# Optimization experiments

Hardware: AMD Instinct MI355X
Metric: run time of the kernel (lower is better)

The kernel has to match this reference:

```python
import jax, jax.numpy as jnp
import numpy as np

_EPS = 1e-5

def _bn(x, g, t, m, v):
    # inference-mode BatchNorm (channels-last)
    return g * (x - m) * jax.lax.rsqrt(v + _EPS) + t

def _lin(x, w, b):
    # 1x1 conv == linear over last (channel) axis; w: (out, in)
    return jnp.einsum('...c,oc->...o', x, w) + b

def _forward(points, k, c0_w, c0_b, c0_g, c0_t, c0_m, c0_v,
             c1_w, c1_b, c1_g, c1_t, c1_m, c1_v,
             a0_w, a0_b, a0_g, a0_t, a0_m, a0_v,
             a1_w, a1_b, a1_g, a1_t, a1_m, a1_v,
             a2_w, a2_b, a2_g, a2_t, a2_m, a2_v,
             c2_w, c2_b, c2_g, c2_t, c2_m, c2_v,
             c3_w, c3_b, c3_g, c3_t, c3_m, c3_v,
             c4_w, c4_b):
    B, N, _ = points.shape
    # per-point MLP: 3 -> 64 -> 64
    x = jax.nn.relu(_bn(_lin(points, c0_w, c0_b), c0_g, c0_t, c0_m, c0_v))
    x = jax.nn.relu(_bn(_lin(x, c1_w, c1_b), c1_g, c1_t, c1_m, c1_v))
    # kNN via squared distances (same ordering as cdist); idx: (B,N,k)
    sq = jnp.sum(points * points, axis=-1)  # (B,N)
    d = sq[:, :, None] + sq[:, None, :] - 2.0 * jnp.einsum('bnc,bmc->bnm', points, points)
    idx = jax.lax.top_k(-d, k)[1]  # (B,N,k) smallest distances
    bidx = jnp.arange(B)[:, None, None]
    grouped_xyz = points[bidx, idx] - points[:, :, None, :]  # (B,N,k,3), centered
    grouped_pts = x[bidx, idx]                                # (B,N,k,64)
    g = jnp.concatenate([grouped_xyz, grouped_pts], axis=-1)  # (B,N,k,67)
    # per-neighbor MLP 67 -> 64 -> 128 -> 128
    for (w, b, ga, t, m, v) in ((a0_w, a0_b, a0_g, a0_t, a0_m, a0_v),
                                (a1_w, a1_b, a1_g, a1_t, a1_m, a1_v),
                                (a2_w, a2_b, a2_g, a2_t, a2_m, a2_v)):
        g = jax.nn.relu(_bn(_lin(g, w, b), ga, t, m, v))
    local = jnp.max(g, axis=2)                 # (B,N,128) max over k neighbors
    gf = jnp.max(local, axis=1, keepdims=True)  # (B,1,128) global feature
    feat = jnp.concatenate([local, jnp.broadcast_to(gf, local.shape)], axis=-1)  # (B,N,256)
    feat = jax.nn.relu(_bn(_lin(feat, c2_w, c2_b), c2_g, c2_t, c2_m, c2_v))
    feat = jax.nn.relu(_bn(_lin(feat, c3_w, c3_b), c3_g, c3_t, c3_m, c3_v))
    # dropout is identity in eval mode
    return _lin(feat, c4_w, c4_b)  # (B,N,6)

def setup_inputs() -> dict:
    key = jax.random.key(0)
    B, N, K = 8, 4096, 16
    specs = [("c0", 64, 3, True), ("c1", 64, 64, True), ("a0", 64, 67, True),
             ("a1", 128, 64, True), ("a2", 128, 128, True), ("c2", 256, 256, True),
             ("c3", 128, 256, True), ("c4", 6, 128, False)]
    inp = {"points": jax.random.normal(key, (B, N, 3), jnp.float32)}
    i = 0
    for name, o, c, has_bn in specs:
        i += 1
        kw = jax.random.fold_in(key, i)
        inp[name + "_w"] = jax.random.normal(kw, (o, c), jnp.float32) * 0.05
        inp[name + "_b"] = jnp.zeros((o,), jnp.float32)
        if has_bn:
            inp[name + "_g"] = jnp.ones((o,), jnp.float32)
            inp[name + "_t"] = jnp.zeros((o,), jnp.float32)
            inp[name + "_m"] = jax.random.normal(jax.random.fold_in(kw, 1), (o,), jnp.float32) * 0.05
            inp[name + "_v"] = jnp.ones((o,), jnp.float32)
    inp["k"] = K
    return inp

def reference(points, c0_w, c0_b, c0_g, c0_t, c0_m, c0_v,
              c1_w, c1_b, c1_g, c1_t, c1_m, c1_v,
              a0_w, a0_b, a0_g, a0_t, a0_m, a0_v,
              a1_w, a1_b, a1_g, a1_t, a1_m, a1_v,
              a2_w, a2_b, a2_g, a2_t, a2_m, a2_v,
              c2_w, c2_b, c2_g, c2_t, c2_m, c2_v,
              c3_w, c3_b, c3_g, c3_t, c3_m, c3_v,
              c4_w, c4_b, k):
    return _forward(points, k, c0_w, c0_b, c0_g, c0_t, c0_m, c0_v,
                    c1_w, c1_b, c1_g, c1_t, c1_m, c1_v,
                    a0_w, a0_b, a0_g, a0_t, a0_m, a0_v,
                    a1_w, a1_b, a1_g, a1_t, a1_m, a1_v,
                    a2_w, a2_b, a2_g, a2_t, a2_m, a2_v,
                    c2_w, c2_b, c2_g, c2_t, c2_m, c2_v,
                    c3_w, c3_b, c3_g, c3_t, c3_m, c3_v,
                    c4_w, c4_b)
```

## Files before the change

### kernel.cpp

```cpp
#include <hip/hip_runtime.h>
#include <math.h>


#define EPSBN 1e-5f

typedef _Float16 v8h  __attribute__((ext_vector_type(8)));
typedef _Float16 v4h  __attribute__((ext_vector_type(4)));
typedef float    v16f __attribute__((ext_vector_type(16)));

#define W0T_OFF   0
#define B0_OFF    192
#define W1T_OFF   256
#define B1_OFF    4352
#define A0XT_OFF  4416
#define A0FT_OFF  4608
#define BA0_OFF   8704
#define A1T_OFF   8768
#define BA1_OFF   16960
#define A2T_OFF   17088
#define BA2_OFF   33472
#define C2T_OFF   33600
#define C3H_OFF   66368
#define BC2_OFF   99136
#define BC3_OFF   132160
#define C4T_OFF   132288
#define BC4_OFF   133056
#define PTS4_OFF  133120
#define Q_OFF     264192
#define C_OFF     2361344
#define IDX_OFF   4458496
#define LOCAL_OFF 4982784
#define GF_OFF    9177088

__device__ __forceinline__ void fold_one(int e, const float* w, const float* b,
    const float* g, const float* t, const float* m, const float* v,
    float* wt, float* bo, int O, int Cfull, int cbeg)
{
    int o = e % O, c = e / O;
    float s = 1.0f;
    if (g) s = g[o] * (1.0f / sqrtf(v[o] + EPSBN));
    wt[c * O + o] = w[o * Cfull + cbeg + c] * s;
    if (c == 0 && bo) {
        float bias = b[o];
        if (g) bias = (bias - m[o]) * s + t[o];
        bo[o] = bias;
    }
}

__global__ __launch_bounds__(256) void fold_kernel(
    const float* c0w, const float* c0b, const float* c0g, const float* c0t, const float* c0m, const float* c0v,
    const float* c1w, const float* c1b, const float* c1g, const float* c1t, const float* c1m, const float* c1v,
    const float* a0w, const float* a0b, const float* a0g, const float* a0t, const float* a0m, const float* a0v,
    const float* a1w, const float* a1b, const float* a1g, const float* a1t, const float* a1m, const float* a1v,
    const float* a2w, const float* a2b, const float* a2g, const float* a2t, const float* a2m, const float* a2v,
    const float* c2w, const float* c2b, const float* c2g, const float* c2t, const float* c2m, const float* c2v,
    const float* c3w, const float* c3b, const float* c3g, const float* c3t, const float* c3m, const float* c3v,
    const float* c4w, const float* c4b,
    float* ws)
{
    int e = blockIdx.x * 256 + threadIdx.x;
    if (e < 192)        { fold_one(e,          c0w, c0b, c0g, c0t, c0m, c0v, ws + W0T_OFF,  ws + B0_OFF,  64, 3,   0); return; }
    e -= 192;
    if (e < 4096)       { fold_one(e,          c1w, c1b, c1g, c1t, c1m, c1v, ws + W1T_OFF,  ws + B1_OFF,  64, 64,  0); return; }
    e -= 4096;
    if (e < 192)        { fold_one(e,          a0w, a0b, a0g, a0t, a0m, a0v, ws + A0XT_OFF, ws + BA0_OFF, 64, 67,  0); return; }
    e -= 192;
    if (e < 4096)       { fold_one(e,          a0w, a0b, a0g, a0t, a0m, a0v, ws + A0FT_OFF, nullptr,      64, 67,  3); return; }
    e -= 4096;
    if (e < 8192) {
        int j = e & 7, l = (e >> 3) & 63, kf = (e >> 9) & 3, wv = e >> 11;
        int o = wv * 32 + (l & 31);
        int c = kf * 16 + (l >> 5) * 8 + j;
        float s = a1g[o] * (1.0f / sqrtf(a1v[o] + EPSBN));
        ((_Float16*)(ws + A1T_OFF))[e] = (_Float16)(a1w[o * 64 + c] * s);
        if (c == 0) ws[BA1_OFF + o] = (a1b[o] - a1m[o]) * s + a1t[o];
        return;
    }
    e -= 8192;
    if (e < 16384) {
        int j = e & 7, l = (e >> 3) & 63, kf = (e >> 9) & 7, wv = e >> 12;
        int o = wv * 32 + (l & 31);
        int c = kf * 16 + (l >> 5) * 8 + j;
        float s = a2g[o] * (1.0f / sqrtf(a2v[o] + EPSBN));
        ((_Float16*)(ws + A2T_OFF))[e] = (_Float16)(a2w[o * 128 + c] * s);
        if (c == 0) ws[BA2_OFF + o] = (a2b[o] - a2m[o]) * s + a2t[o];
        return;
    }
    e -= 16384;
    if (e < 65536) {
        int j = e & 7, l = (e >> 3) & 63, s5 = (e >> 9) & 15, ot = e >> 13;
        int o = ot * 32 + (l & 31);
        int c = s5 * 16 + (l >> 5) * 8 + j;
        float sc = c2g[o] * (1.0f / sqrtf(c2v[o] + EPSBN));
        ((_Float16*)(ws + C2T_OFF))[e] = (_Float16)(c2w[o * 256 + c] * sc);
        if (c == 0) ws[BC2_OFF + o] = (c2b[o] - c2m[o]) * sc + c2t[o];
        return;
    }
    e -= 65536;
    if (e < 32768) {
        int j = e & 7, l = (e >> 3) & 63, s5 = (e >> 9) & 15, ot = e >> 13;
        int o = ot * 32 + (l & 31);
        int c = s5 * 16 + (l >> 5) * 8 + j;
        float sc = c3g[o] * (1.0f / sqrtf(c3v[o] + EPSBN));
        ((_Float16*)(ws + C3H_OFF))[e] = (_Float16)(c3w[o * 256 + c] * sc);
        if (c == 0) ws[BC3_OFF + o] = (c3b[o] - c3m[o]) * sc + c3t[o];
        return;
    }
    e -= 32768;
    if (e < 768)        { fold_one(e,          c4w, c4b, nullptr, nullptr, nullptr, nullptr, ws + C4T_OFF, ws + BC4_OFF, 6, 128, 0); return; }
    e -= 768;
    if (e < 1024)       { ws[GF_OFF + e] = 0.0f; return; }
}

__global__ __launch_bounds__(256) void point_mlp_kernel(const float* __restrict__ pts, float* __restrict__ ws)
{
    __shared__ float sh[4][64][4];
    __shared__ float sx[4][64][4];
    int lane = threadIdx.x & 63;
    int wv = threadIdx.x >> 6;
    int pid0 = blockIdx.x * 16 + wv * 4;

    const float* pc = pts + (size_t)pid0 * 3;
    float c0x = pc[0], c0y = pc[1],  c0z = pc[2];
    float c1x = pc[3], c1y = pc[4],  c1z = pc[5];
    float c2x = pc[6], c2y = pc[7],  c2z = pc[8];
    float c3x = pc[9], c3y = pc[10], c3z = pc[11];

    if (lane < 4) {
        const float* pp = pts + (size_t)(pid0 + lane) * 3;
        float xx = pp[0], yy = pp[1], zz = pp[2];
        float sq = __fadd_rn(__fadd_rn(__fmul_rn(xx, xx), __fmul_rn(yy, yy)), __fmul_rn(zz, zz));
        ((float4*)(ws + PTS4_OFF))[pid0 + lane] = make_float4(xx, yy, zz, sq);
    }

    const float* W0T  = ws + W0T_OFF;
    const float* B0   = ws + B0_OFF;
    const float* W1T  = ws + W1T_OFF;
    const float* B1   = ws + B1_OFF;
    const float* A0XT = ws + A0XT_OFF;
    const float* A0FT = ws + A0FT_OFF;
    const float* BA0  = ws + BA0_OFF;

    float b0 = B0[lane];
    float w0a = W0T[lane], w0b = W0T[64 + lane], w0c = W0T[128 + lane];
    float4 h;
    h.x = fmaxf(fmaf(c0z, w0c, fmaf(c0y, w0b, fmaf(c0x, w0a, b0))), 0.0f);
    h.y = fmaxf(fmaf(c1z, w0c, fmaf(c1y, w0b, fmaf(c1x, w0a, b0))), 0.0f);
    h.z = fmaxf(fmaf(c2z, w0c, fmaf(c2y, w0b, fmaf(c2x, w0a, b0))), 0.0f);
    h.w = fmaxf(fmaf(c3z, w0c, fmaf(c3y, w0b, fmaf(c3x, w0a, b0))), 0.0f);
    *(float4*)&sh[wv][lane][0] = h;

    float b1v = B1[lane];
    float a0 = b1v, a1 = b1v, a2 = b1v, a3 = b1v;
    #pragma unroll 8
    for (int c = 0; c < 64; ++c) {
        float w = W1T[c * 64 + lane];
        float4 hv = *(const float4*)&sh[wv][c][0];
        a0 = fmaf(w, hv.x, a0);
        a1 = fmaf(w, hv.y, a1);
        a2 = fmaf(w, hv.z, a2);
        a3 = fmaf(w, hv.w, a3);
    }
    float4 xv;
    xv.x = fmaxf(a0, 0.0f);
    xv.y = fmaxf(a1, 0.0f);
    xv.z = fmaxf(a2, 0.0f);
    xv.w = fmaxf(a3, 0.0f);
    *(float4*)&sx[wv][lane][0] = xv;

    float ax = A0XT[lane], ay = A0XT[64 + lane], az = A0XT[128 + lane];
    float q0 = __fmul_rn(c0x, ax); q0 = fmaf(c0y, ay, q0); q0 = fmaf(c0z, az, q0);
    float q1 = __fmul_rn(c1x, ax); q1 = fmaf(c1y, ay, q1); q1 = fmaf(c1z, az, q1);
    float q2 = __fmul_rn(c2x, ax); q2 = fmaf(c2y, ay, q2); q2 = fmaf(c2z, az, q2);
    float q3 = __fmul_rn(c3x, ax); q3 = fmaf(c3y, ay, q3); q3 = fmaf(c3z, az, q3);
    ws[Q_OFF + (size_t)(pid0 + 0) * 64 + lane] = q0;
    ws[Q_OFF + (size_t)(pid0 + 1) * 64 + lane] = q1;
    ws[Q_OFF + (size_t)(pid0 + 2) * 64 + lane] = q2;
    ws[Q_OFF + (size_t)(pid0 + 3) * 64 + lane] = q3;

    float ba = BA0[lane];
    float e0 = q0 + ba, e1 = q1 + ba, e2 = q2 + ba, e3 = q3 + ba;
    #pragma unroll 8
    for (int c = 0; c < 64; ++c) {
        float w = A0FT[c * 64 + lane];
        float4 sv = *(const float4*)&sx[wv][c][0];
        e0 = fmaf(w, sv.x, e0);
        e1 = fmaf(w, sv.y, e1);
        e2 = fmaf(w, sv.z, e2);
        e3 = fmaf(w, sv.w, e3);
    }
    ws[C_OFF + (size_t)(pid0 + 0) * 64 + lane] = e0;
    ws[C_OFF + (size_t)(pid0 + 1) * 64 + lane] = e1;
    ws[C_OFF + (size_t)(pid0 + 2) * 64 + lane] = e2;
    ws[C_OFF + (size_t)(pid0 + 3) * 64 + lane] = e3;
}

__device__ __forceinline__ float dist2_ref(float xn, float yn, float zn, float sqn, float4 pm)
{
    float dot = __fmul_rn(xn, pm.x);
    dot = __fmaf_rn(yn, pm.y, dot);
    dot = __fmaf_rn(zn, pm.z, dot);
    float s = __fadd_rn(sqn, pm.w);
    return __fmaf_rn(-2.0f, dot, s);
}

__device__ __forceinline__ float dtilde(float xn, float yn, float zn, float4 pm)
{
    float dot = __fmul_rn(xn, pm.x);
    dot = __fmaf_rn(yn, pm.y, dot);
    dot = __fmaf_rn(zn, pm.z, dot);
    return __fmaf_rn(-2.0f, dot, pm.w);
}

#define KNN_CAP 64
#define KNN_MARGIN 1e-3f

__device__ __forceinline__ void knn_row(
    const float4* __restrict__ pts4, int* __restrict__ IDX,
    float* __restrict__ bufdW, int* __restrict__ bufiW, int* __restrict__ cntp,
    int base, int rbase, int rw, int l, float gm, float tvd)
{
    unsigned long long qm = __ballot(gm <= tvd);

    float4 pr = pts4[rbase + rw];
    float xr = pr.x, yr = pr.y, zr = pr.z, sr = pr.w;
    float tve = __fadd_rn(sr, tvd);

    int cr = 0;
    #define KNN_PROC(GG, CV)                                                   \
    {                                                                          \
        float d = dist2_ref(xr, yr, zr, sr, (CV));                             \
        bool p = (d <= tve);                                                   \
        unsigned long long mk = __ballot(p);                                   \
        int my = __builtin_amdgcn_mbcnt_hi((unsigned)(mk >> 32),               \
                 __builtin_amdgcn_mbcnt_lo((unsigned)mk, 0));                  \
        int slot = cr + my;                                                    \
        if (p && slot < KNN_CAP) { bufdW[slot] = d; bufiW[slot] = (GG) * 64 + l; } \
        cr += (int)__popcll(mk);                                               \
    }
    while (qm) {
        int g0 = __ffsll((unsigned long long)qm) - 1; qm &= qm - 1;
        int g1 = -1, g2 = -1, g3 = -1;
        if (qm) { g1 = __ffsll((unsigned long long)qm) - 1; qm &= qm - 1;
            if (qm) { g2 = __ffsll((unsigned long long)qm) - 1; qm &= qm - 1;
                if (qm) { g3 = __ffsll((unsigned long long)qm) - 1; qm &= qm - 1; } } }
        float4 cv0 = pts4[base + g0 * 64 + l];
        float4 cv1, cv2, cv3;
        if (g1 >= 0) cv1 = pts4[base + g1 * 64 + l];
        if (g2 >= 0) cv2 = pts4[base + g2 * 64 + l];
        if (g3 >= 0) cv3 = pts4[base + g3 * 64 + l];
        KNN_PROC(g0, cv0);
        if (g1 >= 0) KNN_PROC(g1, cv1);
        if (g2 >= 0) KNN_PROC(g2, cv2);
        if (g3 >= 0) KNN_PROC(g3, cv3);
    }
    #undef KNN_PROC
    if (l == 0) *cntp = cr;

    if (cr <= KNN_CAP) {
        unsigned long long key = ~0ULL;
        if (l < cr) {
            unsigned u = __float_as_uint(bufdW[l]);
            u = (u & 0x80000000u) ? ~u : (u | 0x80000000u);
            key = ((unsigned long long)u << 32) | (unsigned)bufiW[l];
        }
        if (cr <= 32) {
            #pragma unroll
            for (int k = 2; k <= 32; k <<= 1) {
                #pragma unroll
                for (int j = k >> 1; j > 0; j >>= 1) {
                    unsigned long long o = __shfl_xor(key, j);
                    bool mx = (((l & j) != 0) == ((l & k) == 0));
                    key = mx ? (key > o ? key : o) : (key < o ? key : o);
                }
            }
        } else {
            #pragma unroll
            for (int k = 2; k <= 64; k <<= 1) {
                #pragma unroll
                for (int j = k >> 1; j > 0; j >>= 1) {
                    unsigned long long o = __shfl_xor(key, j);
                    bool mx = (((l & j) != 0) == ((l & k) == 0));
                    key = mx ? (key > o ? key : o) : (key < o ? key : o);
                }
            }
        }
        if (l < 16)
            IDX[(rbase + rw) * 16 + l] = (int)(key & 0xFFFFFFFFu);
    }
}

__global__ __launch_bounds__(1024) void knn_kernel(float* __restrict__ ws)
{
    __shared__ float gmins[64 * 65];
    __shared__ float bufd[16][72];
    __shared__ int   bufi[16][72];
    __shared__ int   cnt[64];

    const float4* __restrict__ pts4 = (const float4*)(ws + PTS4_OFF);
    int* IDX = (int*)(ws + IDX_OFF);

    const int l     = threadIdx.x & 63;
    const int row   = l;
    const int wvu   = __builtin_amdgcn_readfirstlane(threadIdx.x >> 6);
    const int base  = (blockIdx.x >> 6) << 12;
    const int rbase = blockIdx.x * 64;
    const int r     = rbase + row;

    float4 pn = pts4[r];
    float xn = pn.x, yn = pn.y, zn = pn.z, sqn = pn.w;
    (void)sqn;

    #pragma unroll
    for (int g = 0; g < 4; ++g) {
        const float4* __restrict__ cp = pts4 + base + wvu * 256 + g * 64;
        float mn0 = INFINITY, mn1 = INFINITY, mn2 = INFINITY, mn3 = INFINITY;
        #pragma unroll 4
        for (int i = 0; i < 64; i += 4) {
            mn0 = fminf(mn0, dtilde(xn, yn, zn, cp[i + 0]));
            mn1 = fminf(mn1, dtilde(xn, yn, zn, cp[i + 1]));
            mn2 = fminf(mn2, dtilde(xn, yn, zn, cp[i + 2]));
            mn3 = fminf(mn3, dtilde(xn, yn, zn, cp[i + 3]));
        }
        gmins[row * 65 + wvu * 4 + g] = fminf(fminf(mn0, mn1), fminf(mn2, mn3));
    }
    __syncthreads();

    float gm0 = gmins[(wvu * 4 + 0) * 65 + l];
    float gm1 = gmins[(wvu * 4 + 1) * 65 + l];
    float gm2 = gmins[(wvu * 4 + 2) * 65 + l];
    float gm3 = gmins[(wvu * 4 + 3) * 65 + l];
    float v0 = gm0, v1 = gm1, v2 = gm2, v3 = gm3;
    #pragma unroll
    for (int k = 2; k <= 64; k <<= 1) {
        #pragma unroll
        for (int j = k >> 1; j > 0; j >>= 1) {
            float o0 = __shfl_xor(v0, j);
            float o1 = __shfl_xor(v1, j);
            float o2 = __shfl_xor(v2, j);
            float o3 = __shfl_xor(v3, j);
            bool mx = (((l & j) != 0) == ((l & k) == 0));
            v0 = mx ? fmaxf(v0, o0) : fminf(v0, o0);
            v1 = mx ? fmaxf(v1, o1) : fminf(v1, o1);
            v2 = mx ? fmaxf(v2, o2) : fminf(v2, o2);
            v3 = mx ? fmaxf(v3, o3) : fminf(v3, o3);
        }
    }
    float tvd0 = __shfl(v0, 16) + KNN_MARGIN;
    float tvd1 = __shfl(v1, 16) + KNN_MARGIN;
    float tvd2 = __shfl(v2, 16) + KNN_MARGIN;
    float tvd3 = __shfl(v3, 16) + KNN_MARGIN;

    knn_row(pts4, IDX, bufd[wvu], bufi[wvu], &cnt[wvu * 4 + 0], base, rbase, wvu * 4 + 0, l, gm0, tvd0);
    knn_row(pts4, IDX, bufd[wvu], bufi[wvu], &cnt[wvu * 4 + 1], base, rbase, wvu * 4 + 1, l, gm1, tvd1);
    knn_row(pts4, IDX, bufd[wvu], bufi[wvu], &cnt[wvu * 4 + 2], base, rbase, wvu * 4 + 2, l, gm2, tvd2);
    knn_row(pts4, IDX, bufd[wvu], bufi[wvu], &cnt[wvu * 4 + 3], base, rbase, wvu * 4 + 3, l, gm3, tvd3);
    __syncthreads();

    if (threadIdx.x < 64 && cnt[threadIdx.x] > KNN_CAP) {
        int* out = IDX + (rbase + threadIdx.x) * 16;
        float hd[16]; int hi[16];
        #pragma unroll
        for (int t2 = 0; t2 < 16; ++t2) { hd[t2] = INFINITY; hi[t2] = 0; }
        for (int mm = 0; mm < 4096; ++mm) {
            float d = dist2_ref(xn, yn, zn, pn.w, pts4[base + mm]);
            if (d < hd[15]) {
                float vd = d; int vi = mm;
                #pragma unroll
                for (int t2 = 0; t2 < 16; ++t2) {
                    bool sm = vd < hd[t2];
                    float td = hd[t2]; int ti = hi[t2];
                    if (sm) { hd[t2] = vd; hi[t2] = vi; vd = td; vi = ti; }
                }
            }
        }
        for (int jj = 0; jj < 16; ++jj) out[jj] = hi[jj];
    }
}

__device__ __forceinline__ float max16_dpp(float v)
{
    int vi = __float_as_int(v);
    v = fmaxf(v, __int_as_float(__builtin_amdgcn_update_dpp(0, vi, 0xB1, 0xf, 0xf, true)));
    vi = __float_as_int(v);
    v = fmaxf(v, __int_as_float(__builtin_amdgcn_update_dpp(0, vi, 0x4E, 0xf, 0xf, true)));
    vi = __float_as_int(v);
    v = fmaxf(v, __int_as_float(__builtin_amdgcn_update_dpp(0, vi, 0x141, 0xf, 0xf, true)));
    vi = __float_as_int(v);
    v = fmaxf(v, __int_as_float(__builtin_amdgcn_update_dpp(0, vi, 0x140, 0xf, 0xf, true)));
    return v;
}

__device__ __forceinline__ void nbr_stage_g1(
    _Float16* sG1, const float* Cf, const float* Qf,
    int t, int gpt0, int g, int base, int m)
{
    int r = t >> 2, cs = t & 3;
    int gpt = gpt0 + g * 4 + (r >> 4);
    const float4* crow = (const float4*)(Cf + (size_t)(base + m) * 64) + cs * 4;
    const float4* qrow = (const float4*)(Qf + (size_t)gpt * 64) + cs * 4;
    v8h h0, h1;
    #pragma unroll
    for (int u = 0; u < 2; ++u) {
        float4 cv = crow[u], qv = qrow[u];
        h0[u * 4 + 0] = (_Float16)fmaxf(cv.x - qv.x, 0.0f);
        h0[u * 4 + 1] = (_Float16)fmaxf(cv.y - qv.y, 0.0f);
        h0[u * 4 + 2] = (_Float16)fmaxf(cv.z - qv.z, 0.0f);
        h0[u * 4 + 3] = (_Float16)fmaxf(cv.w - qv.w, 0.0f);
    }
    #pragma unroll
    for (int u = 0; u < 2; ++u) {
        float4 cv = crow[2 + u], qv = qrow[2 + u];
        h1[u * 4 + 0] = (_Float16)fmaxf(cv.x - qv.x, 0.0f);
        h1[u * 4 + 1] = (_Float16)fmaxf(cv.y - qv.y, 0.0f);
        h1[u * 4 + 2] = (_Float16)fmaxf(cv.z - qv.z, 0.0f);
        h1[u * 4 + 3] = (_Float16)fmaxf(cv.w - qv.w, 0.0f);
    }
    int rs = r & 7;
    *(v8h*)&sG1[r * 64 + ((cs * 2    ) ^ rs) * 8] = h0;
    *(v8h*)&sG1[r * 64 + ((cs * 2 + 1) ^ rs) * 8] = h1;
}

__global__ __launch_bounds__(256) void nbr_mlp_mfma_kernel(float* __restrict__ ws)
{
    __shared__ __align__(16) unsigned char smem[33792];
    _Float16* sG1   = (_Float16*)smem;
    _Float16* sH1   = (_Float16*)(smem + 8192);
    float*    sPool = (float*)(smem + 24576);
    float*    sB1   = (float*)(smem + 32768);
    float*    sB2   = (float*)(smem + 33280);

    const int t   = threadIdx.x;
    const int l   = t & 63;
    const int w   = t >> 6;
    const int ln  = l & 31;
    const int hi  = l >> 5;
    const int blk = blockIdx.x;
    const int gpt0 = blk * 16;
    const int base = (blk >> 8) << 12;

    const float* Cf = ws + C_OFF;
    const float* Qf = ws + Q_OFF;
    const int* IDX = (const int*)(ws + IDX_OFF);

    if (t < 128) sB1[t] = ws[BA1_OFF + t];
    else         sB2[t - 128] = ws[BA2_OFF + (t - 128)];

    int mi[4];
    {
        int r = t >> 2;
        #pragma unroll
        for (int g = 0; g < 4; ++g)
            mi[g] = IDX[(gpt0 + g * 4 + (r >> 4)) * 16 + (r & 15)];
    }

    v8h fa[4], fa2[8];
    {
        const float4* a1img = (const float4*)(ws + A1T_OFF);
        const float4* a2img = (const float4*)(ws + A2T_OFF);
        #pragma unroll
        for (int kf = 0; kf < 4; ++kf) {
            float4 tmp = a1img[(w * 4 + kf) * 64 + l];
            fa[kf] = *(v8h*)&tmp;
        }
        #pragma unroll
        for (int kf = 0; kf < 8; ++kf) {
            float4 tmp = a2img[(w * 8 + kf) * 64 + l];
            fa2[kf] = *(v8h*)&tmp;
        }
    }

    nbr_stage_g1(sG1, Cf, Qf, t, gpt0, 0, base, mi[0]);
    __syncthreads();

    for (int g = 0; g < 4; ++g) {
        #pragma unroll
        for (int rt = 0; rt < 2; ++rt) {
            int r = rt * 32 + ln, rs = r & 7;
            v16f acc;
            #pragma unroll
            for (int i = 0; i < 16; ++i) acc[i] = 0.0f;
            #pragma unroll
            for (int kf = 0; kf < 4; ++kf) {
                v8h fb = *(const v8h*)&sG1[r * 64 + ((kf * 2 + hi) ^ rs) * 8];
                acc = __builtin_amdgcn_mfma_f32_32x32x16_f16(fa[kf], fb, acc, 0, 0, 0);
            }
            #pragma unroll
            for (int q = 0; q < 4; ++q) {
                float4 b4 = *(const float4*)&sB1[w * 32 + 8 * q + 4 * hi];
                v4h hv;
                hv[0] = (_Float16)fmaxf(acc[q * 4 + 0] + b4.x, 0.0f);
                hv[1] = (_Float16)fmaxf(acc[q * 4 + 1] + b4.y, 0.0f);
                hv[2] = (_Float16)fmaxf(acc[q * 4 + 2] + b4.z, 0.0f);
                hv[3] = (_Float16)fmaxf(acc[q * 4 + 3] + b4.w, 0.0f);
                int gg = w * 4 + q;
                *(v4h*)&sH1[r * 128 + ((gg ^ rs) * 8) + 4 * hi] = hv;
            }
        }
        __syncthreads();

        if (g < 3) nbr_stage_g1(sG1, Cf, Qf, t, gpt0, g + 1, base, mi[g + 1]);

        #pragma unroll
        for (int rt = 0; rt < 2; ++rt) {
            int r = rt * 32 + ln, rs = r & 7;
            v16f acc;
            #pragma unroll
            for (int i = 0; i < 16; ++i) acc[i] = 0.0f;
            #pragma unroll
            for (int kf = 0; kf < 8; ++kf) {
                v8h fb = *(const v8h*)&sH1[r * 128 + ((kf * 2 + hi) ^ rs) * 8];
                acc = __builtin_amdgcn_mfma_f32_32x32x16_f16(fa2[kf], fb, acc, 0, 0, 0);
            }
            #pragma unroll
            for (int i = 0; i < 16; ++i) acc[i] = max16_dpp(acc[i]);
            if ((l & 15) == 0) {
                int p = g * 4 + rt * 2 + ((l >> 4) & 1);
                #pragma unroll
                for (int q = 0; q < 4; ++q) {
                    float4 b4 = *(const float4*)&sB2[w * 32 + 8 * q + 4 * hi];
                    float4 o4;
                    o4.x = fmaxf(acc[q * 4 + 0] + b4.x, 0.0f);
                    o4.y = fmaxf(acc[q * 4 + 1] + b4.y, 0.0f);
                    o4.z = fmaxf(acc[q * 4 + 2] + b4.z, 0.0f);
                    o4.w = fmaxf(acc[q * 4 + 3] + b4.w, 0.0f);
                    int ob = w * 32 + 8 * q + 4 * hi;
                    *(float4*)&sPool[p * 128 + ob] = o4;
                }
            }
        }
        __syncthreads();
    }

    {
        float* LOCAL = ws + LOCAL_OFF;
        const float4* sp4 = (const float4*)sPool;
        #pragma unroll
        for (int u = 0; u < 2; ++u) {
            int e = t + 256 * u;
            int pp = e >> 5, cc = e & 31;
            ((float4*)&LOCAL[(size_t)(gpt0 + pp) * 128])[cc] = sp4[e];
        }
    }

    if (t < 128) {
        float m = 0.0f;
        #pragma unroll
        for (int p = 0; p < 16; ++p) m = fmaxf(m, sPool[p * 128 + t]);
        atomicMax((int*)(ws + GF_OFF) + (blk >> 8) * 128 + t, __float_as_int(m));
    }
}

__global__ __launch_bounds__(256) void head_mfma_kernel(float* __restrict__ ws, float* __restrict__ out)
{
    __shared__ __align__(16) unsigned char smem[66560];
    _Float16* sF  = (_Float16*)smem;
    float*    sF3 = (float*)smem;
    _Float16* sF2 = (_Float16*)(smem + 33792);

    const int t  = threadIdx.x;
    const int l  = t & 63;
    const int w  = t >> 6;
    const int ln = l & 31;
    const int hi = l >> 5;
    const int gpt0 = blockIdx.x * 64;
    const int b = blockIdx.x >> 6;

    const float4* c2h = (const float4*)(ws + C2T_OFF);
    const float4* c3h = (const float4*)(ws + C3H_OFF);

    {
        int m = t >> 2, cs = t & 3;
        const float4* src = (cs < 2)
            ? (const float4*)(ws + LOCAL_OFF + (size_t)(gpt0 + m) * 128) + cs * 16
            : (const float4*)(ws + GF_OFF + b * 128) + (cs - 2) * 16;
        int c0 = cs * 64;
        #pragma unroll
        for (int u = 0; u < 8; ++u) {
            float4 a0 = src[u * 2], a1 = src[u * 2 + 1];
            v8h h;
            h[0] = (_Float16)a0.x; h[1] = (_Float16)a0.y;
            h[2] = (_Float16)a0.z; h[3] = (_Float16)a0.w;
            h[4] = (_Float16)a1.x; h[5] = (_Float16)a1.y;
            h[6] = (_Float16)a1.z; h[7] = (_Float16)a1.w;
            int g = ((c0 >> 3) + u) ^ (m & 31);
            *(v8h*)&sF[m * 256 + g * 8] = h;
        }
    }
    __syncthreads();

    #pragma unroll
    for (int ot = 0; ot < 2; ++ot) {
        int ot2 = 2 * w + ot;
        v8h fa[16];
        #pragma unroll
        for (int s = 0; s < 16; ++s) {
            float4 tmp = c2h[(ot2 * 16 + s) * 64 + l];
            fa[s] = *(v8h*)&tmp;
        }
        float b2[16];
        #pragma unroll
        for (int i = 0; i < 16; ++i)
            b2[i] = ws[BC2_OFF + ot2 * 32 + (i & 3) + 8 * (i >> 2) + 4 * hi];
        #pragma unroll
        for (int mt = 0; mt < 2; ++mt) {
            int m = mt * 32 + ln;
            v16f acc;
            #pragma unroll
            for (int i = 0; i < 16; ++i) acc[i] = 0.0f;
            #pragma unroll
            for (int s = 0; s < 16; ++s) {
                v8h fb = *(const v8h*)&sF[m * 256 + (((2 * s + hi) ^ ln) * 8)];
                acc = __builtin_amdgcn_mfma_f32_32x32x16_f16(fa[s], fb, acc, 0, 0, 0);
            }
            #pragma unroll
            for (int q = 0; q < 4; ++q) {
                v4h hv;
                #pragma unroll
                for (int j = 0; j < 4; ++j)
                    hv[j] = (_Float16)fmaxf(acc[q * 4 + j] + b2[q * 4 + j], 0.0f);
                *(v4h*)&sF2[m * 256 + (((ot2 * 4 + q) ^ ln) * 8) + 4 * hi] = hv;
            }
        }
    }
    __syncthreads();

    {
        v8h fa[16];
        #pragma unroll
        for (int s = 0; s < 16; ++s) {
            float4 tmp = c3h[(w * 16 + s) * 64 + l];
            fa[s] = *(v8h*)&tmp;
        }
        float b3[16];
        #pragma unroll
        for (int i = 0; i < 16; ++i)
            b3[i] = ws[BC3_OFF + w * 32 + (i & 3) + 8 * (i >> 2) + 4 * hi];
        #pragma unroll
        for (int mt = 0; mt < 2; ++mt) {
            int m = mt * 32 + ln;
            v16f acc;
            #pragma unroll
            for (int i = 0; i < 16; ++i) acc[i] = 0.0f;
            #pragma unroll
            for (int s = 0; s < 16; ++s) {
                v8h fb = *(const v8h*)&sF2[m * 256 + (((2 * s + hi) ^ ln) * 8)];
                acc = __builtin_amdgcn_mfma_f32_32x32x16_f16(fa[s], fb, acc, 0, 0, 0);
            }
            #pragma unroll
            for (int q = 0; q < 4; ++q) {
                float4 hv;
                hv.x = fmaxf(acc[q * 4 + 0] + b3[q * 4 + 0], 0.0f);
                hv.y = fmaxf(acc[q * 4 + 1] + b3[q * 4 + 1], 0.0f);
                hv.z = fmaxf(acc[q * 4 + 2] + b3[q * 4 + 2], 0.0f);
                hv.w = fmaxf(acc[q * 4 + 3] + b3[q * 4 + 3], 0.0f);
                *(float4*)&sF3[m * 132 + w * 32 + q * 8 + 4 * hi] = hv;
            }
        }
    }
    __syncthreads();

    const float* C4T = ws + C4T_OFF;
    for (int mo = t; mo < 384; mo += 256) {
        int m = mo / 6, o = mo - m * 6;
        float a = ws[BC4_OFF + o];
        const float4* f4 = (const float4*)(sF3 + m * 132);
        #pragma unroll 8
        for (int kq = 0; kq < 32; ++kq) {
            float4 f = f4[kq];
            a = fmaf(f.x, C4T[(kq * 4 + 0) * 6 + o], a);
            a = fmaf(f.y, C4T[(kq * 4 + 1) * 6 + o], a);
            a = fmaf(f.z, C4T[(kq * 4 + 2) * 6 + o], a);
            a = fmaf(f.w, C4T[(kq * 4 + 3) * 6 + o], a);
        }
        out[(size_t)(gpt0 + m) * 6 + o] = a;
    }
}

extern "C" void kernel_launch(void* const* d_in, const int* in_sizes, int n_in,
                              void* d_out, int out_size, void* d_ws, size_t ws_size,
                              hipStream_t stream)
{
    const float* pts = (const float*)d_in[0];
    float* ws = (float*)d_ws;
    float* out = (float*)d_out;

    fold_kernel<<<521, 256, 0, stream>>>(
        (const float*)d_in[1],  (const float*)d_in[2],  (const float*)d_in[3],  (const float*)d_in[4],  (const float*)d_in[5],  (const float*)d_in[6],
        (const float*)d_in[7],  (const float*)d_in[8],  (const float*)d_in[9],  (const float*)d_in[10], (const float*)d_in[11], (const float*)d_in[12],
        (const float*)d_in[13], (const float*)d_in[14], (const float*)d_in[15], (const float*)d_in[16], (const float*)d_in[17], (const float*)d_in[18],
        (const float*)d_in[19], (const float*)d_in[20], (const float*)d_in[21], (const float*)d_in[22], (const float*)d_in[23], (const float*)d_in[24],
        (const float*)d_in[25], (const float*)d_in[26], (const float*)d_in[27], (const float*)d_in[28], (const float*)d_in[29], (const float*)d_in[30],
        (const float*)d_in[31], (const float*)d_in[32], (const float*)d_in[33], (const float*)d_in[34], (const float*)d_in[35], (const float*)d_in[36],
        (const float*)d_in[37], (const float*)d_in[38], (const float*)d_in[39], (const float*)d_in[40], (const float*)d_in[41], (const float*)d_in[42],
        (const float*)d_in[43], (const float*)d_in[44],
        ws);

    point_mlp_kernel<<<2048, 256, 0, stream>>>(pts, ws);
    knn_kernel<<<512, 1024, 0, stream>>>(ws);
    nbr_mlp_mfma_kernel<<<2048, 256, 0, stream>>>(ws);
    head_mfma_kernel<<<512, 256, 0, stream>>>(ws, out);
}
```

Before: 312.0 us.

## Split kNN into group-min pass and per-row selection pass with smaller blocks

The single 1024-thread kNN kernel becomes two kernels. The first computes per-64-column-group minimum distances with 256-thread blocks and writes them transposed to global workspace, reusing the LOCAL region. The second loads a 16-row tile of those minima, derives thresholds and runs the row selection with 256-thread blocks. This aims for better occupancy and load balance than 1024-thread blocks, at the cost of an extra launch and a global round trip for the group minima.

```diff
diff --git a/kernel.cpp b/kernel.cpp
--- a/kernel.cpp
+++ b/kernel.cpp
@@ -31,6 +31,7 @@
 #define IDX_OFF   4458496
 #define LOCAL_OFF 4982784
 #define GF_OFF    9177088
+#define GMINS_OFF LOCAL_OFF
 
 __device__ __forceinline__ void fold_one(int e, const float* w, const float* b,
     const float* g, const float* t, const float* m, const float* v,
@@ -290,30 +291,25 @@
     }
 }
 
-__global__ __launch_bounds__(1024) void knn_kernel(float* __restrict__ ws)
-{
-    __shared__ float gmins[64 * 65];
-    __shared__ float bufd[16][72];
-    __shared__ int   bufi[16][72];
-    __shared__ int   cnt[64];
-
+__global__ __launch_bounds__(256) void knn_p1_kernel(float* __restrict__ ws)
+{
     const float4* __restrict__ pts4 = (const float4*)(ws + PTS4_OFF);
-    int* IDX = (int*)(ws + IDX_OFF);
-
-    const int l     = threadIdx.x & 63;
-    const int row   = l;
-    const int wvu   = __builtin_amdgcn_readfirstlane(threadIdx.x >> 6);
-    const int base  = (blockIdx.x >> 6) << 12;
-    const int rbase = blockIdx.x * 64;
-    const int r     = rbase + row;
-
-    float4 pn = pts4[r];
-    float xn = pn.x, yn = pn.y, zn = pn.z, sqn = pn.w;
-    (void)sqn;
+    float* __restrict__ gminsT = ws + GMINS_OFF;
+
+    const int l        = threadIdx.x & 63;
+    const int wvu      = __builtin_amdgcn_readfirstlane(threadIdx.x >> 6);
+    const int colchunk = blockIdx.x & 3;
+    const int rowblock = blockIdx.x >> 2;
+    const int base     = (rowblock >> 6) << 12;
+    const int rbase    = rowblock * 64;
+
+    float4 pn = pts4[rbase + l];
+    float xn = pn.x, yn = pn.y, zn = pn.z;
 
     #pragma unroll
     for (int g = 0; g < 4; ++g) {
-        const float4* __restrict__ cp = pts4 + base + wvu * 256 + g * 64;
+        const int col = colchunk * 16 + wvu * 4 + g;
+        const float4* __restrict__ cp = pts4 + base + col * 64;
         float mn0 = INFINITY, mn1 = INFINITY, mn2 = INFINITY, mn3 = INFINITY;
         #pragma unroll 4
         for (int i = 0; i < 64; i += 4) {
@@ -322,14 +318,39 @@
             mn2 = fminf(mn2, dtilde(xn, yn, zn, cp[i + 2]));
             mn3 = fminf(mn3, dtilde(xn, yn, zn, cp[i + 3]));
         }
-        gmins[row * 65 + wvu * 4 + g] = fminf(fminf(mn0, mn1), fminf(mn2, mn3));
+        gminsT[col * 32768 + rbase + l] = fminf(fminf(mn0, mn1), fminf(mn2, mn3));
+    }
+}
+
+__global__ __launch_bounds__(256) void knn_p2_kernel(float* __restrict__ ws)
+{
+    __shared__ float tile[64 * 17];
+    __shared__ float bufd[4][72];
+    __shared__ int   bufi[4][72];
+    __shared__ int   cnt[16];
+
+    const float4* __restrict__ pts4 = (const float4*)(ws + PTS4_OFF);
+    const float* __restrict__ gminsT = ws + GMINS_OFF;
+    int* IDX = (int*)(ws + IDX_OFF);
+
+    const int t     = threadIdx.x;
+    const int l     = t & 63;
+    const int wvu   = __builtin_amdgcn_readfirstlane(t >> 6);
+    const int rbase = blockIdx.x * 16;
+    const int base  = (blockIdx.x >> 8) << 12;
+
+    #pragma unroll
+    for (int u = 0; u < 4; ++u) {
+        int e = t + 256 * u;
+        int col = e >> 4, rr = e & 15;
+        tile[col * 17 + rr] = gminsT[col * 32768 + rbase + rr];
     }
     __syncthreads();
 
-    float gm0 = gmins[(wvu * 4 + 0) * 65 + l];
-    float gm1 = gmins[(wvu * 4 + 1) * 65 + l];
-    float gm2 = gmins[(wvu * 4 + 2) * 65 + l];
-    float gm3 = gmins[(wvu * 4 + 3) * 65 + l];
+    float gm0 = tile[l * 17 + wvu * 4 + 0];
+    float gm1 = tile[l * 17 + wvu * 4 + 1];
+    float gm2 = tile[l * 17 + wvu * 4 + 2];
+    float gm3 = tile[l * 17 + wvu * 4 + 3];
     float v0 = gm0, v1 = gm1, v2 = gm2, v3 = gm3;
     #pragma unroll
     for (int k = 2; k <= 64; k <<= 1) {
@@ -357,13 +378,16 @@
     knn_row(pts4, IDX, bufd[wvu], bufi[wvu], &cnt[wvu * 4 + 3], base, rbase, wvu * 4 + 3, l, gm3, tvd3);
     __syncthreads();
 
-    if (threadIdx.x < 64 && cnt[threadIdx.x] > KNN_CAP) {
-        int* out = IDX + (rbase + threadIdx.x) * 16;
+    if (t < 16 && cnt[t] > KNN_CAP) {
+        int row = rbase + t;
+        float4 pn = pts4[row];
+        float xn = pn.x, yn = pn.y, zn = pn.z, sqn = pn.w;
+        int* out = IDX + row * 16;
         float hd[16]; int hi[16];
         #pragma unroll
         for (int t2 = 0; t2 < 16; ++t2) { hd[t2] = INFINITY; hi[t2] = 0; }
         for (int mm = 0; mm < 4096; ++mm) {
-            float d = dist2_ref(xn, yn, zn, pn.w, pts4[base + mm]);
+            float d = dist2_ref(xn, yn, zn, sqn, pts4[base + mm]);
             if (d < hd[15]) {
                 float vd = d; int vi = mm;
                 #pragma unroll
@@ -697,7 +721,8 @@
         ws);
 
     point_mlp_kernel<<<2048, 256, 0, stream>>>(pts, ws);
-    knn_kernel<<<512, 1024, 0, stream>>>(ws);
+    knn_p1_kernel<<<2048, 256, 0, stream>>>(ws);
+    knn_p2_kernel<<<2048, 256, 0, stream>>>(ws);
     nbr_mlp_mfma_kernel<<<2048, 256, 0, stream>>>(ws);
     head_mfma_kernel<<<512, 256, 0, stream>>>(ws, out);
 }
```

Result: slower. 336.3 us (+7.8%).
